# Kernel optimization log

Hardware: AMD Instinct MI355X
Metric: run time of the kernel (lower is better)

## Reference

```python
import jax, jax.numpy as jnp
import numpy as np
from jax.experimental.jet import jet

ORDER = 3  # Taylor order from init_kwargs
D, C, H = 4096, 4096, 8192


def setup_inputs() -> dict:
    key = jax.random.key(0)
    k = jax.random.split(key, 6)
    sc1 = 1.0 / np.sqrt(D + C)
    sc2 = 1.0 / np.sqrt(H)
    return {
        "h": jax.random.normal(k[0], (D,), jnp.float32),
        "r": jnp.zeros((), jnp.float32),  # ignored residual slot of h_r tuple
        "t": jax.random.uniform(k[1], (), jnp.float32),
        "c": jax.random.normal(k[2], (C,), jnp.float32),
        "W1": jax.random.normal(k[3], (D + C, H), jnp.float32) * sc1,
        "b1": jnp.zeros((H,), jnp.float32),
        "W2": jax.random.normal(k[4], (H, D), jnp.float32) * sc2,
        "b2": jnp.zeros((D,), jnp.float32),
    }


def reference(h, r, t, c, W1, b1, W2, b2):
    # dynamics f(h, t, c): 2-layer tanh MLP on concat(h, c)
    def f(_h, _t, _c):
        x = jnp.concatenate((_h, _c))
        return jnp.tanh(x @ W1 + b1) @ W2 + b2

    h_shape = h.shape

    def g(h_t):
        # expand flattened state+time through dynamics
        _h, _t = jnp.reshape(h_t[:-1], h_shape), h_t[-1]
        dh = jnp.ravel(f(_h, _t, c))
        return jnp.concatenate((dh, jnp.array([1.0], dtype=dh.dtype)))

    h_t = jnp.concatenate((jnp.ravel(h), jnp.reshape(t, (1,))))
    # recursive Taylor-mode jet expansion
    (y0, [*yns]) = jet(g, (h_t,), ((jnp.ones_like(h_t),),))
    for _ in range(ORDER - 1):
        (y0, [*yns]) = jet(g, (h_t,), ((y0, *yns),))
    dydt = jnp.reshape(y0[:-1], h_shape)
    drdt = jnp.reshape(yns[-2][:-1], h_shape)
    return (dydt, jnp.mean(drdt ** 2))
```

## Files before the change

kernel.cpp:

```cpp
#include <hip/hip_runtime.h>

#define DD 4096
#define HH 8192

enum Stage { S_X0 = 0, S_TANH, S_BIASOUT, S_PMUL, S_COPY, S_S2 };

template <int STAGE, int KS, int SPREV, int KPREV, int NTOT, int CPT>
__global__ __launch_bounds__(256) void gemv_stage(
    const float* __restrict__ W,
    const float* __restrict__ Pprev,
    float* __restrict__ Pout,
    const float* __restrict__ h, const float* __restrict__ c,
    const float* __restrict__ b1, const float* __restrict__ b2,
    float* __restrict__ s0g, float* __restrict__ t0g, float* __restrict__ a1g,
    float* __restrict__ outv)
{
    constexpr int GROUPS = 256 / KS;
    __shared__ float xs[KS];
    __shared__ float part[GROUPS][KS];

    const int tid = threadIdx.x;
    const int k0 = blockIdx.y * KS;

    if constexpr (STAGE == S_X0) {
        if (tid < KS) {
            int k = k0 + tid;
            xs[tid] = (k < DD) ? h[k] : c[k - DD];
        }
    } else {
        const int g = tid / KS;
        const int j = tid % KS;
        float acc = 0.f;
        for (int s = g; s < SPREV; s += GROUPS)
            acc += Pprev[(size_t)s * KPREV + k0 + j];
        part[g][j] = acc;
        __syncthreads();
        if (tid < KS) {
            const int k = k0 + tid;
            float tot = 0.f;
#pragma unroll
            for (int g2 = 0; g2 < GROUPS; ++g2) tot += part[g2][tid];
            float xv;
            if constexpr (STAGE == S_TANH) {
                float s = tanhf(tot + b1[k]);
                float t = 1.f - s * s;
                xv = s;
                if (blockIdx.x == 0) { s0g[k] = s; t0g[k] = t; }
            } else if constexpr (STAGE == S_BIASOUT) {
                xv = tot + b2[k];
                if (blockIdx.x == 0) outv[k] = xv;
            } else if constexpr (STAGE == S_PMUL) {
                xv = t0g[k] * tot;
                if (blockIdx.x == 0) a1g[k] = tot;
            } else if constexpr (STAGE == S_COPY) {
                xv = tot;
            } else {
                float a1v = a1g[k];
                xv = t0g[k] * (tot - s0g[k] * a1v * a1v);
            }
            xs[tid] = xv;
        }
    }
    __syncthreads();

    if constexpr (CPT == 4) {
        const int ncol = blockIdx.x * 1024 + tid * 4;
        const float* Wp = W + (size_t)k0 * NTOT + ncol;
        float ax = 0.f, ay = 0.f, az = 0.f, aw = 0.f;
#pragma unroll 8
        for (int k = 0; k < KS; ++k) {
            float xv = xs[k];
            float4 w = *reinterpret_cast<const float4*>(Wp + (size_t)k * NTOT);
            ax = fmaf(xv, w.x, ax);
            ay = fmaf(xv, w.y, ay);
            az = fmaf(xv, w.z, az);
            aw = fmaf(xv, w.w, aw);
        }
        *reinterpret_cast<float4*>(Pout + (size_t)blockIdx.y * NTOT + ncol) =
            make_float4(ax, ay, az, aw);
    } else {
        const int ncol = blockIdx.x * 512 + tid * 2;
        const float* Wp = W + (size_t)k0 * NTOT + ncol;
        float ax = 0.f, ay = 0.f;
#pragma unroll 8
        for (int k = 0; k < KS; ++k) {
            float xv = xs[k];
            float2 w = *reinterpret_cast<const float2*>(Wp + (size_t)k * NTOT);
            ax = fmaf(xv, w.x, ax);
            ay = fmaf(xv, w.y, ay);
        }
        *reinterpret_cast<float2*>(Pout + (size_t)blockIdx.y * NTOT + ncol) =
            make_float2(ax, ay);
    }
}

__global__ __launch_bounds__(256) void reduce_C2(const float* __restrict__ P6,
                                                 float* __restrict__ C2) {
    int n = blockIdx.x * 256 + threadIdx.x;
    float acc = 0.f;
#pragma unroll 8
    for (int s = 0; s < 128; ++s) acc += P6[(size_t)s * DD + n];
    C2[n] = acc;
}

__global__ __launch_bounds__(256) void reduce_meansq(const float* __restrict__ C2v,
                                                     float* __restrict__ dout) {
    float s = 0.f;
    for (int i = threadIdx.x; i < DD; i += 256) {
        float v = C2v[i];
        s = fmaf(v, v, s);
    }
    for (int off = 32; off; off >>= 1) s += __shfl_down(s, off);
    __shared__ float ls[4];
    int wid = threadIdx.x >> 6;
    if ((threadIdx.x & 63) == 0) ls[wid] = s;
    __syncthreads();
    if (threadIdx.x == 0) {
        dout[DD] = (ls[0] + ls[1] + ls[2] + ls[3]) / (float)DD;
    }
}

extern "C" void kernel_launch(void* const* d_in, const int* in_sizes, int n_in,
                              void* d_out, int out_size, void* d_ws, size_t ws_size,
                              hipStream_t stream) {
    const float* h  = (const float*)d_in[0];
    const float* c  = (const float*)d_in[3];
    const float* W1 = (const float*)d_in[4];
    const float* b1 = (const float*)d_in[5];
    const float* W2 = (const float*)d_in[6];
    const float* b2 = (const float*)d_in[7];
    float* out = (float*)d_out;
    float* ws = (float*)d_ws;

    float* P1 = ws;
    float* P2 = P1 + 1048576;
    float* P3 = P2 + 524288;
    float* P4 = P3 + 1048576;
    float* P5 = P4 + 524288;
    float* P6 = P5 + 1048576;
    float* s0 = P6 + 524288;
    float* t0 = s0 + 8192;
    float* a1 = t0 + 8192;
    float* C2 = a1 + 8192;

    gemv_stage<S_X0, 64, 1, 1, HH, 4><<<dim3(8, 128), 256, 0, stream>>>(
        W1, nullptr, P1, h, c, b1, b2, s0, t0, a1, out);
    gemv_stage<S_TANH, 64, 128, HH, DD, 2><<<dim3(8, 128), 256, 0, stream>>>(
        W2, P1, P2, h, c, b1, b2, s0, t0, a1, out);
    gemv_stage<S_BIASOUT, 32, 128, DD, HH, 4><<<dim3(8, 128), 256, 0, stream>>>(
        W1, P2, P3, h, c, b1, b2, s0, t0, a1, out);
    gemv_stage<S_PMUL, 64, 128, HH, DD, 2><<<dim3(8, 128), 256, 0, stream>>>(
        W2, P3, P4, h, c, b1, b2, s0, t0, a1, out);
    gemv_stage<S_COPY, 32, 128, DD, HH, 4><<<dim3(8, 128), 256, 0, stream>>>(
        W1, P4, P5, h, c, b1, b2, s0, t0, a1, out);
    gemv_stage<S_S2, 64, 128, HH, DD, 2><<<dim3(8, 128), 256, 0, stream>>>(
        W2, P5, P6, h, c, b1, b2, s0, t0, a1, out);
    reduce_C2<<<16, 256, 0, stream>>>(P6, C2);
    reduce_meansq<<<1, 256, 0, stream>>>(C2, out);
}
```

Baseline: 214.6 us.

## Convert weights to bf16 during first pass and use bf16 GEMVs afterward

The first two GEMV stages, which read fp32 W1 and W2, now also write bf16 copies of the rows they touch into workspace. The four later stages read these bf16 copies, halving their weight traffic, and widen to four columns per thread with fewer column blocks on the W2 stages. This adds bf16 write traffic in the first two stages and reduces accuracy of the later Taylor terms. The conversion is redone on every call, so nothing is reused across calls.

Measured after the change: 237.9 us. 10.8% more time.

```diff
diff --git a/kernel.cpp b/kernel.cpp
--- a/kernel.cpp
+++ b/kernel.cpp
@@ -2,23 +2,27 @@
 
 #define DD 4096
 #define HH 8192
+#define NSPLIT 128
 
 enum Stage { S_X0 = 0, S_TANH, S_BIASOUT, S_PMUL, S_COPY, S_S2 };
 
+__device__ inline unsigned short f2bf(float f) {
+    unsigned int u = __float_as_uint(f);
+    u += 0x7FFFu + ((u >> 16) & 1u);
+    return (unsigned short)(u >> 16);
+}
+
 template <int STAGE, int KS, int SPREV, int KPREV, int NTOT, int CPT>
-__global__ __launch_bounds__(256) void gemv_stage(
-    const float* __restrict__ W,
-    const float* __restrict__ Pprev,
-    float* __restrict__ Pout,
+__global__ __launch_bounds__(256) void gemv_f32(
+    const float* __restrict__ W, const float* __restrict__ Pprev,
+    float* __restrict__ Pout, unsigned short* __restrict__ Wb, int convRows,
     const float* __restrict__ h, const float* __restrict__ c,
-    const float* __restrict__ b1, const float* __restrict__ b2,
-    float* __restrict__ s0g, float* __restrict__ t0g, float* __restrict__ a1g,
-    float* __restrict__ outv)
+    const float* __restrict__ b1,
+    float* __restrict__ s0g, float* __restrict__ t0g)
 {
     constexpr int GROUPS = 256 / KS;
     __shared__ float xs[KS];
     __shared__ float part[GROUPS][KS];
-
     const int tid = threadIdx.x;
     const int k0 = blockIdx.y * KS;
 
@@ -40,13 +44,85 @@
             float tot = 0.f;
 #pragma unroll
             for (int g2 = 0; g2 < GROUPS; ++g2) tot += part[g2][tid];
+            float s = tanhf(tot + b1[k]);
+            xs[tid] = s;
+            if (blockIdx.x == 0) { s0g[k] = s; t0g[k] = 1.f - s * s; }
+        }
+    }
+    __syncthreads();
+
+    const bool doConv = (k0 < convRows);
+
+    if constexpr (CPT == 4) {
+        const int ncol = blockIdx.x * 1024 + tid * 4;
+        const float* Wp = W + (size_t)k0 * NTOT + ncol;
+        float ax = 0.f, ay = 0.f, az = 0.f, aw = 0.f;
+#pragma unroll 4
+        for (int k = 0; k < KS; ++k) {
+            float xv = xs[k];
+            float4 w = *reinterpret_cast<const float4*>(Wp + (size_t)k * NTOT);
+            ax = fmaf(xv, w.x, ax);
+            ay = fmaf(xv, w.y, ay);
+            az = fmaf(xv, w.z, az);
+            aw = fmaf(xv, w.w, aw);
+            if (doConv) {
+                ushort4 o;
+                o.x = f2bf(w.x); o.y = f2bf(w.y); o.z = f2bf(w.z); o.w = f2bf(w.w);
+                *reinterpret_cast<ushort4*>(Wb + (size_t)(k0 + k) * NTOT + ncol) = o;
+            }
+        }
+        *reinterpret_cast<float4*>(Pout + (size_t)blockIdx.y * NTOT + ncol) =
+            make_float4(ax, ay, az, aw);
+    } else {
+        const int ncol = blockIdx.x * 512 + tid * 2;
+        const float* Wp = W + (size_t)k0 * NTOT + ncol;
+        float ax = 0.f, ay = 0.f;
+#pragma unroll 4
+        for (int k = 0; k < KS; ++k) {
+            float xv = xs[k];
+            float2 w = *reinterpret_cast<const float2*>(Wp + (size_t)k * NTOT);
+            ax = fmaf(xv, w.x, ax);
+            ay = fmaf(xv, w.y, ay);
+            if (doConv) {
+                ushort2 o;
+                o.x = f2bf(w.x); o.y = f2bf(w.y);
+                *reinterpret_cast<ushort2*>(Wb + (size_t)(k0 + k) * NTOT + ncol) = o;
+            }
+        }
+        *reinterpret_cast<float2*>(Pout + (size_t)blockIdx.y * NTOT + ncol) =
+            make_float2(ax, ay);
+    }
+}
+
+template <int STAGE, int KS, int SPREV, int KPREV, int NTOT>
+__global__ __launch_bounds__(256) void gemv_b16(
+    const unsigned short* __restrict__ Wb, const float* __restrict__ Pprev,
+    float* __restrict__ Pout,
+    const float* __restrict__ b2, const float* __restrict__ s0g,
+    const float* __restrict__ t0g, float* __restrict__ a1g,
+    float* __restrict__ outv)
+{
+    constexpr int GROUPS = 256 / KS;
+    __shared__ float xs[KS];
+    __shared__ float part[GROUPS][KS];
+    const int tid = threadIdx.x;
+    const int k0 = blockIdx.y * KS;
+
+    {
+        const int g = tid / KS;
+        const int j = tid % KS;
+        float acc = 0.f;
+        for (int s = g; s < SPREV; s += GROUPS)
+            acc += Pprev[(size_t)s * KPREV + k0 + j];
+        part[g][j] = acc;
+        __syncthreads();
+        if (tid < KS) {
+            const int k = k0 + tid;
+            float tot = 0.f;
+#pragma unroll
+            for (int g2 = 0; g2 < GROUPS; ++g2) tot += part[g2][tid];
             float xv;
-            if constexpr (STAGE == S_TANH) {
-                float s = tanhf(tot + b1[k]);
-                float t = 1.f - s * s;
-                xv = s;
-                if (blockIdx.x == 0) { s0g[k] = s; t0g[k] = t; }
-            } else if constexpr (STAGE == S_BIASOUT) {
+            if constexpr (STAGE == S_BIASOUT) {
                 xv = tot + b2[k];
                 if (blockIdx.x == 0) outv[k] = xv;
             } else if constexpr (STAGE == S_PMUL) {
@@ -63,35 +139,24 @@
     }
     __syncthreads();
 
-    if constexpr (CPT == 4) {
-        const int ncol = blockIdx.x * 1024 + tid * 4;
-        const float* Wp = W + (size_t)k0 * NTOT + ncol;
-        float ax = 0.f, ay = 0.f, az = 0.f, aw = 0.f;
+    const int ncol = blockIdx.x * 1024 + tid * 4;
+    const unsigned short* Wp = Wb + (size_t)k0 * NTOT + ncol;
+    float ax = 0.f, ay = 0.f, az = 0.f, aw = 0.f;
 #pragma unroll 8
-        for (int k = 0; k < KS; ++k) {
-            float xv = xs[k];
-            float4 w = *reinterpret_cast<const float4*>(Wp + (size_t)k * NTOT);
-            ax = fmaf(xv, w.x, ax);
-            ay = fmaf(xv, w.y, ay);
-            az = fmaf(xv, w.z, az);
-            aw = fmaf(xv, w.w, aw);
-        }
-        *reinterpret_cast<float4*>(Pout + (size_t)blockIdx.y * NTOT + ncol) =
-            make_float4(ax, ay, az, aw);
-    } else {
-        const int ncol = blockIdx.x * 512 + tid * 2;
-        const float* Wp = W + (size_t)k0 * NTOT + ncol;
-        float ax = 0.f, ay = 0.f;
-#pragma unroll 8
-        for (int k = 0; k < KS; ++k) {
-            float xv = xs[k];
-            float2 w = *reinterpret_cast<const float2*>(Wp + (size_t)k * NTOT);
-            ax = fmaf(xv, w.x, ax);
-            ay = fmaf(xv, w.y, ay);
-        }
-        *reinterpret_cast<float2*>(Pout + (size_t)blockIdx.y * NTOT + ncol) =
-            make_float2(ax, ay);
-    }
+    for (int k = 0; k < KS; ++k) {
+        float xv = xs[k];
+        uint2 w = *reinterpret_cast<const uint2*>(Wp + (size_t)k * NTOT);
+        float w0 = __uint_as_float(w.x << 16);
+        float w1 = __uint_as_float(w.x & 0xFFFF0000u);
+        float w2 = __uint_as_float(w.y << 16);
+        float w3 = __uint_as_float(w.y & 0xFFFF0000u);
+        ax = fmaf(xv, w0, ax);
+        ay = fmaf(xv, w1, ay);
+        az = fmaf(xv, w2, az);
+        aw = fmaf(xv, w3, aw);
+    }
+    *reinterpret_cast<float4*>(Pout + (size_t)blockIdx.y * NTOT + ncol) =
+        make_float4(ax, ay, az, aw);
 }
 
 __global__ __launch_bounds__(256) void reduce_C2(const float* __restrict__ P6,
@@ -99,7 +164,7 @@
     int n = blockIdx.x * 256 + threadIdx.x;
     float acc = 0.f;
 #pragma unroll 8
-    for (int s = 0; s < 128; ++s) acc += P6[(size_t)s * DD + n];
+    for (int s = 0; s < NSPLIT; ++s) acc += P6[(size_t)s * DD + n];
     C2[n] = acc;
 }
 
@@ -115,9 +180,7 @@
     int wid = threadIdx.x >> 6;
     if ((threadIdx.x & 63) == 0) ls[wid] = s;
     __syncthreads();
-    if (threadIdx.x == 0) {
-        dout[DD] = (ls[0] + ls[1] + ls[2] + ls[3]) / (float)DD;
-    }
+    if (threadIdx.x == 0) dout[DD] = (ls[0] + ls[1] + ls[2] + ls[3]) / (float)DD;
 }
 
 extern "C" void kernel_launch(void* const* d_in, const int* in_sizes, int n_in,
@@ -142,19 +205,21 @@
     float* t0 = s0 + 8192;
     float* a1 = t0 + 8192;
     float* C2 = a1 + 8192;
-
-    gemv_stage<S_X0, 64, 1, 1, HH, 4><<<dim3(8, 128), 256, 0, stream>>>(
-        W1, nullptr, P1, h, c, b1, b2, s0, t0, a1, out);
-    gemv_stage<S_TANH, 64, 128, HH, DD, 2><<<dim3(8, 128), 256, 0, stream>>>(
-        W2, P1, P2, h, c, b1, b2, s0, t0, a1, out);
-    gemv_stage<S_BIASOUT, 32, 128, DD, HH, 4><<<dim3(8, 128), 256, 0, stream>>>(
-        W1, P2, P3, h, c, b1, b2, s0, t0, a1, out);
-    gemv_stage<S_PMUL, 64, 128, HH, DD, 2><<<dim3(8, 128), 256, 0, stream>>>(
-        W2, P3, P4, h, c, b1, b2, s0, t0, a1, out);
-    gemv_stage<S_COPY, 32, 128, DD, HH, 4><<<dim3(8, 128), 256, 0, stream>>>(
-        W1, P4, P5, h, c, b1, b2, s0, t0, a1, out);
-    gemv_stage<S_S2, 64, 128, HH, DD, 2><<<dim3(8, 128), 256, 0, stream>>>(
-        W2, P5, P6, h, c, b1, b2, s0, t0, a1, out);
+    unsigned short* W1b = (unsigned short*)(C2 + 4096);
+    unsigned short* W2b = W1b + (size_t)DD * HH;
+
+    gemv_f32<S_X0, 64, 1, 1, HH, 4><<<dim3(8, NSPLIT), 256, 0, stream>>>(
+        W1, nullptr, P1, W1b, DD, h, c, b1, s0, t0);
+    gemv_f32<S_TANH, 64, NSPLIT, HH, DD, 2><<<dim3(8, NSPLIT), 256, 0, stream>>>(
+        W2, P1, P2, W2b, HH, h, c, b1, s0, t0);
+    gemv_b16<S_BIASOUT, 32, NSPLIT, DD, HH><<<dim3(8, NSPLIT), 256, 0, stream>>>(
+        W1b, P2, P3, b2, s0, t0, a1, out);
+    gemv_b16<S_PMUL, 64, NSPLIT, HH, DD><<<dim3(4, NSPLIT), 256, 0, stream>>>(
+        W2b, P3, P4, b2, s0, t0, a1, out);
+    gemv_b16<S_COPY, 32, NSPLIT, DD, HH><<<dim3(8, NSPLIT), 256, 0, stream>>>(
+        W1b, P4, P5, b2, s0, t0, a1, out);
+    gemv_b16<S_S2, 64, NSPLIT, HH, DD><<<dim3(4, NSPLIT), 256, 0, stream>>>(
+        W2b, P5, P6, b2, s0, t0, a1, out);
     reduce_C2<<<16, 256, 0, stream>>>(P6, C2);
     reduce_meansq<<<1, 256, 0, stream>>>(C2, out);
 }
```
